# Optimization experiments

Measured on AMD Instinct MI355X. Metric: run time of the kernel, lower is better.

The kernel has to match this reference:

```python
import jax, jax.numpy as jnp
import numpy as np

D_MODEL = 1024
NUM_HEADS = 16
HEAD_DIM = D_MODEL // NUM_HEADS


def setup_inputs() -> dict:
    key = jax.random.key(0)
    ks = jax.random.split(key, 9)
    s = 1.0 / np.sqrt(D_MODEL)  # torch Linear default init range scale
    def lin(k):
        kw, kb = jax.random.split(k)
        W = jax.random.uniform(kw, (D_MODEL, D_MODEL), jnp.float32, -s, s)
        b = jax.random.uniform(kb, (D_MODEL,), jnp.float32, -s, s)
        return W, b
    Wq, bq = lin(ks[0])
    Wk, bk = lin(ks[1])
    Wv, bv = lin(ks[2])
    Wo, bo = lin(ks[3])
    x = jax.random.normal(ks[4], (4, 2048, D_MODEL), jnp.float32)
    return {"x": x, "Wq": Wq, "bq": bq, "Wk": Wk, "bk": bk,
            "Wv": Wv, "bv": bv, "Wo": Wo, "bo": bo}


def reference(x, Wq, bq, Wk, bk, Wv, bv, Wo, bo):
    B, S, _ = x.shape
    H, Dh = NUM_HEADS, HEAD_DIM
    scale = Dh ** -0.5
    # projections; W stored as [in, out] so y = x @ W + b
    q = (x @ Wq + bq).reshape(B, S, H, Dh).transpose(0, 2, 1, 3)  # [B,H,S,Dh]
    k = (x @ Wk + bk).reshape(B, S, H, Dh).transpose(0, 2, 1, 3)
    v = (x @ Wv + bv).reshape(B, S, H, Dh).transpose(0, 2, 1, 3)
    scores = jnp.einsum('bhqd,bhkd->bhqk', q, k) * scale  # [B,H,S,S]
    causal = jnp.tril(jnp.ones((S, S), dtype=bool))
    scores = jnp.where(causal[None, None], scores, jnp.finfo(scores.dtype).min)
    attn = jax.nn.softmax(scores, axis=-1)
    out = jnp.einsum('bhqk,bhkd->bhqd', attn, v)  # [B,H,S,Dh]
    out = out.transpose(0, 2, 1, 3).reshape(B, S, H * Dh)
    return out @ Wo + bo
```

## Files before the change

### kernel.cpp

```cpp
#include <hip/hip_runtime.h>
#include <math.h>

#define DM 1024
#define NH 16
#define DH 64
#define BB 4
#define SS 2048
#define MROWS (BB*SS)

typedef __bf16 bf16;
typedef __bf16 bf16x2 __attribute__((ext_vector_type(2)));
typedef __bf16 bf16x8 __attribute__((ext_vector_type(8)));
typedef float floatx4 __attribute__((ext_vector_type(4)));
typedef float floatx16 __attribute__((ext_vector_type(16)));
typedef unsigned int uintx4 __attribute__((ext_vector_type(4)));
typedef unsigned int uintx2 __attribute__((ext_vector_type(2)));

#if __has_builtin(__builtin_amdgcn_exp2f)
#define EXP2F __builtin_amdgcn_exp2f
#else
#define EXP2F exp2f
#endif

#define QSCALE (0.125f * 1.44269504088896f)

__device__ __forceinline__ void cp16(void* lds, const void* g) {
  __builtin_amdgcn_global_load_lds(
      (__attribute__((address_space(1))) void*)(void*)g,
      (__attribute__((address_space(3))) void*)lds,
      16, 0, 0);
}

__device__ __forceinline__ unsigned pk2(float a, float b) {
  bf16x2 t;
  t[0] = (bf16)a;
  t[1] = (bf16)b;
  return __builtin_bit_cast(unsigned, t);
}

#if __has_builtin(__builtin_amdgcn_permlane32_swap)
__device__ __forceinline__ void pl32(unsigned& a, unsigned& b) {
  uintx2 r = __builtin_amdgcn_permlane32_swap(a, b, false, false);
  a = r[0]; b = r[1];
}
#else
__device__ __forceinline__ void pl32(unsigned& a, unsigned& b) {
  asm volatile("v_permlane32_swap_b32 %0, %1" : "+v"(a), "+v"(b));
}
#endif

__global__ __launch_bounds__(256) void cvt_x(
    const float* __restrict__ X, bf16* __restrict__ Y) {
  int i = (blockIdx.x * 256 + threadIdx.x) * 8;
  float4 a = *(const float4*)&X[i];
  float4 b = *(const float4*)&X[i + 4];
  bf16x8 o;
  o[0] = (bf16)a.x; o[1] = (bf16)a.y; o[2] = (bf16)a.z; o[3] = (bf16)a.w;
  o[4] = (bf16)b.x; o[5] = (bf16)b.y; o[6] = (bf16)b.z; o[7] = (bf16)b.w;
  *(bf16x8*)&Y[i] = o;
}

__global__ __launch_bounds__(1024) void wtransc(
    const float* __restrict__ W0, const float* __restrict__ W1,
    const float* __restrict__ W2, const float* __restrict__ W3,
    bf16* __restrict__ T0, bf16* __restrict__ T1,
    bf16* __restrict__ T2, bf16* __restrict__ T3) {
  __shared__ float tile[32][33];
  const float* W; bf16* T;
  int z = blockIdx.z;
  if (z == 0)      { W = W0; T = T0; }
  else if (z == 1) { W = W1; T = T1; }
  else if (z == 2) { W = W2; T = T2; }
  else             { W = W3; T = T3; }
  int tx = threadIdx.x, ty = threadIdx.y;
  tile[ty][tx] = W[(blockIdx.y * 32 + ty) * DM + blockIdx.x * 32 + tx];
  __syncthreads();
  T[(blockIdx.x * 32 + ty) * DM + blockIdx.y * 32 + tx] = (bf16)tile[tx][ty];
}

#define BK 32

__global__ __launch_bounds__(512, 1) void gemm_qkv(
    const bf16* __restrict__ A, const bf16* __restrict__ WT,
    const float* __restrict__ bq, const float* __restrict__ bk,
    const float* __restrict__ bv,
    bf16* __restrict__ qb, bf16* __restrict__ kb, bf16* __restrict__ vt) {
  __shared__ __align__(16) char smem[(2 * 256 * 64 + 2 * 128 * 64) * 2];
  bf16* Ab = (bf16*)smem;
  bf16* Bb = (bf16*)(smem + 2 * 256 * 64 * 2);
  bf16* Ts = (bf16*)smem;

  int tid = threadIdx.x;
  int lane = tid & 63, w = tid >> 6;
  int wr = w >> 1, wc = w & 1;
  int qd = lane >> 4, l15 = lane & 15;

  int bid = blockIdx.x;
  int xcd = bid & 7, local = bid >> 3;
  int nb = local >> 2;
  int mb = xcd * 4 + (local & 3);
  int m0 = mb * 256;
  int n0 = nb * 128;
  int which = n0 >> 10;

  floatx4 acc[4][4] = {};

  auto stageA = [&](int pb, int t, int hf) {
    for (int i = 0; i < 2; ++i) {
      int L = i * 512 + tid;
      int row = L >> 3, ch = L & 7;
      int sch = ch ^ (row & 7);
      cp16(&Ab[pb * 256 * 64 + (hf * 128 + row) * 64 + ch * 8],
           &A[(size_t)(m0 + hf * 128 + row) * DM + t * 64 + sch * 8]);
    }
  };
  auto stageB = [&](int pb, int t) {
    for (int i = 0; i < 2; ++i) {
      int L = i * 512 + tid;
      int row = L >> 3, ch = L & 7;
      int sch = ch ^ (row & 7);
      cp16(&Bb[pb * 128 * 64 + row * 64 + ch * 8],
           &WT[(size_t)(n0 + row) * DM + t * 64 + sch * 8]);
    }
  };
  auto ldA = [&](int pb, int mt, int ks) -> bf16x8 {
    int row = wr * 64 + mt * 16 + l15;
    int c = ((ks << 2) + qd) ^ (row & 7);
    return *(const bf16x8*)&Ab[pb * 256 * 64 + row * 64 + c * 8];
  };
  auto ldB = [&](int pb, int nt, int ks) -> bf16x8 {
    int row = wc * 64 + nt * 16 + l15;
    int c = ((ks << 2) + qd) ^ (row & 7);
    return *(const bf16x8*)&Bb[pb * 128 * 64 + row * 64 + c * 8];
  };

  stageA(0, 0, 0);
  stageA(0, 0, 1);
  stageB(0, 0);
  stageB(1, 1);
  asm volatile("s_waitcnt vmcnt(2)" ::: "memory");
  __builtin_amdgcn_s_barrier();

  for (int g = 0; g < 16; ++g) {
    int pb = g & 1;
    bf16x8 af0[2][2], bfr[4][2];
    for (int mt = 0; mt < 2; ++mt)
      for (int ks = 0; ks < 2; ++ks) af0[mt][ks] = ldA(pb, mt, ks);
    for (int nt = 0; nt < 4; ++nt)
      for (int ks = 0; ks < 2; ++ks) bfr[nt][ks] = ldB(pb, nt, ks);
    if (g + 1 < 16) { stageA(pb ^ 1, g + 1, 0); stageA(pb ^ 1, g + 1, 1); }
    __builtin_amdgcn_s_barrier();
    asm volatile("s_waitcnt lgkmcnt(0)" ::: "memory");
    __builtin_amdgcn_sched_barrier(0);
    __builtin_amdgcn_s_setprio(1);
    for (int mt = 0; mt < 2; ++mt)
      for (int nt = 0; nt < 4; ++nt)
        for (int ks = 0; ks < 2; ++ks)
          acc[mt][nt] = __builtin_amdgcn_mfma_f32_16x16x32_bf16(
              af0[mt][ks], bfr[nt][ks], acc[mt][nt], 0, 0, 0);
    __builtin_amdgcn_s_setprio(0);
    __builtin_amdgcn_s_barrier();
    bf16x8 af1[2][2];
    for (int mt = 0; mt < 2; ++mt)
      for (int ks = 0; ks < 2; ++ks) af1[mt][ks] = ldA(pb, 2 + mt, ks);
    if (g + 2 < 16) stageB(pb, g + 2);
    __builtin_amdgcn_s_barrier();
    asm volatile("s_waitcnt lgkmcnt(0)" ::: "memory");
    __builtin_amdgcn_sched_barrier(0);
    __builtin_amdgcn_s_setprio(1);
    for (int mt = 0; mt < 2; ++mt)
      for (int nt = 0; nt < 4; ++nt)
        for (int ks = 0; ks < 2; ++ks)
          acc[2 + mt][nt] = __builtin_amdgcn_mfma_f32_16x16x32_bf16(
              af1[mt][ks], bfr[nt][ks], acc[2 + mt][nt], 0, 0, 0);
    __builtin_amdgcn_s_setprio(0);
    if (g < 14)
      asm volatile("s_waitcnt vmcnt(2)" ::: "memory");
    else if (g == 14)
      asm volatile("s_waitcnt vmcnt(0)" ::: "memory");
    __builtin_amdgcn_s_barrier();
  }

  __syncthreads();

  const float* bias = (which == 0) ? bq : (which == 1) ? bk : bv;

  if (which == 2) {
    for (int nt = 0; nt < 4; ++nt) {
      int dl = wc * 64 + nt * 16 + l15;
      float bv_ = bias[(n0 & 1023) + dl];
      for (int mt = 0; mt < 4; ++mt)
        for (int r = 0; r < 4; ++r)
          Ts[dl * 264 + wr * 64 + mt * 16 + qd * 4 + r] =
              (bf16)(acc[mt][nt][r] + bv_);
    }
    __syncthreads();
    int dl = tid >> 2, s0 = (tid & 3) * 64;
    size_t vrow = (size_t)((n0 & 1023) + dl) * MROWS + m0 + s0;
    for (int j = 0; j < 8; ++j)
      *(bf16x8*)&vt[vrow + j * 8] = *(const bf16x8*)&Ts[dl * 264 + s0 + j * 8];
  } else {
    bf16* out = (which == 0) ? qb : kb;
    float sc = (which == 0) ? QSCALE : 1.0f;
    for (int nt = 0; nt < 4; ++nt) {
      int col = (n0 & 1023) + wc * 64 + nt * 16 + l15;
      float bv_ = bias[col];
      for (int mt = 0; mt < 4; ++mt)
        for (int r = 0; r < 4; ++r) {
          int row = m0 + wr * 64 + mt * 16 + qd * 4 + r;
          out[(size_t)row * DM + col] = (bf16)((acc[mt][nt][r] + bv_) * sc);
        }
    }
  }
}

__global__ __launch_bounds__(512, 1) void gemm_out(
    const bf16* __restrict__ A, const bf16* __restrict__ WT,
    const float* __restrict__ bias, float* __restrict__ C) {
  __shared__ __align__(16) char smem[(2 * 256 * 64 + 2 * 128 * 64) * 2];
  bf16* Ab = (bf16*)smem;
  bf16* Bb = (bf16*)(smem + 2 * 256 * 64 * 2);

  int tid = threadIdx.x;
  int lane = tid & 63, w = tid >> 6;
  int wr = w >> 1, wc = w & 1;
  int qd = lane >> 4, l15 = lane & 15;

  int bid = blockIdx.x;
  int m0 = (bid >> 3) * 256;
  int n0 = (bid & 7) * 128;

  floatx4 acc[4][4] = {};

  auto stageA = [&](int pb, int t, int hf) {
    for (int i = 0; i < 2; ++i) {
      int L = i * 512 + tid;
      int row = L >> 3, ch = L & 7;
      int sch = ch ^ (row & 7);
      cp16(&Ab[pb * 256 * 64 + (hf * 128 + row) * 64 + ch * 8],
           &A[(size_t)(m0 + hf * 128 + row) * DM + t * 64 + sch * 8]);
    }
  };
  auto stageB = [&](int pb, int t) {
    for (int i = 0; i < 2; ++i) {
      int L = i * 512 + tid;
      int row = L >> 3, ch = L & 7;
      int sch = ch ^ (row & 7);
      cp16(&Bb[pb * 128 * 64 + row * 64 + ch * 8],
           &WT[(size_t)(n0 + row) * DM + t * 64 + sch * 8]);
    }
  };
  auto ldA = [&](int pb, int mt, int ks) -> bf16x8 {
    int row = wr * 64 + mt * 16 + l15;
    int c = ((ks << 2) + qd) ^ (row & 7);
    return *(const bf16x8*)&Ab[pb * 256 * 64 + row * 64 + c * 8];
  };
  auto ldB = [&](int pb, int nt, int ks) -> bf16x8 {
    int row = wc * 64 + nt * 16 + l15;
    int c = ((ks << 2) + qd) ^ (row & 7);
    return *(const bf16x8*)&Bb[pb * 128 * 64 + row * 64 + c * 8];
  };

  stageA(0, 0, 0);
  stageA(0, 0, 1);
  stageB(0, 0);
  stageB(1, 1);
  asm volatile("s_waitcnt vmcnt(2)" ::: "memory");
  __builtin_amdgcn_s_barrier();

  for (int g = 0; g < 16; ++g) {
    int pb = g & 1;
    bf16x8 af0[2][2], bfr[4][2];
    for (int mt = 0; mt < 2; ++mt)
      for (int ks = 0; ks < 2; ++ks) af0[mt][ks] = ldA(pb, mt, ks);
    for (int nt = 0; nt < 4; ++nt)
      for (int ks = 0; ks < 2; ++ks) bfr[nt][ks] = ldB(pb, nt, ks);
    if (g + 1 < 16) { stageA(pb ^ 1, g + 1, 0); stageA(pb ^ 1, g + 1, 1); }
    __builtin_amdgcn_s_barrier();
    asm volatile("s_waitcnt lgkmcnt(0)" ::: "memory");
    __builtin_amdgcn_sched_barrier(0);
    __builtin_amdgcn_s_setprio(1);
    for (int mt = 0; mt < 2; ++mt)
      for (int nt = 0; nt < 4; ++nt)
        for (int ks = 0; ks < 2; ++ks)
          acc[mt][nt] = __builtin_amdgcn_mfma_f32_16x16x32_bf16(
              af0[mt][ks], bfr[nt][ks], acc[mt][nt], 0, 0, 0);
    __builtin_amdgcn_s_setprio(0);
    __builtin_amdgcn_s_barrier();
    bf16x8 af1[2][2];
    for (int mt = 0; mt < 2; ++mt)
      for (int ks = 0; ks < 2; ++ks) af1[mt][ks] = ldA(pb, 2 + mt, ks);
    if (g + 2 < 16) stageB(pb, g + 2);
    __builtin_amdgcn_s_barrier();
    asm volatile("s_waitcnt lgkmcnt(0)" ::: "memory");
    __builtin_amdgcn_sched_barrier(0);
    __builtin_amdgcn_s_setprio(1);
    for (int mt = 0; mt < 2; ++mt)
      for (int nt = 0; nt < 4; ++nt)
        for (int ks = 0; ks < 2; ++ks)
          acc[2 + mt][nt] = __builtin_amdgcn_mfma_f32_16x16x32_bf16(
              af1[mt][ks], bfr[nt][ks], acc[2 + mt][nt], 0, 0, 0);
    __builtin_amdgcn_s_setprio(0);
    if (g < 14)
      asm volatile("s_waitcnt vmcnt(2)" ::: "memory");
    else if (g == 14)
      asm volatile("s_waitcnt vmcnt(0)" ::: "memory");
    __builtin_amdgcn_s_barrier();
  }

  for (int nt = 0; nt < 4; ++nt) {
    int col = n0 + wc * 64 + nt * 16 + l15;
    float bv_ = bias[col];
    for (int mt = 0; mt < 4; ++mt)
      for (int r = 0; r < 4; ++r) {
        int row = m0 + wr * 64 + mt * 16 + qd * 4 + r;
        C[(size_t)row * DM + col] = acc[mt][nt][r] + bv_;
      }
  }
}

__global__ __launch_bounds__(256, 2) void attn_fwd(
    const bf16* __restrict__ Qg, const bf16* __restrict__ Kg,
    const bf16* __restrict__ Vt, bf16* __restrict__ O) {
  __shared__ __align__(16) bf16 Kbuf[3][64 * 64];
  __shared__ __align__(16) bf16 Vbuf[3][64 * 64];

  int tid = threadIdx.x;
  int lane = tid & 63, w = tid >> 6;
  int q31 = lane & 31, hi = lane >> 5;
  int pair = blockIdx.x, h = blockIdx.y, b = blockIdx.z;
  int base = b * SS;
  int hoff = h * DH;

  auto stage = [&](int bi, int kt) {
    int kbase = base + kt * 64;
    for (int i = 0; i < 2; ++i) {
      int c = i * 256 + tid;
      int row = c >> 3;
      int sch = (c & 7) ^ (row & 7);
      cp16(&Kbuf[bi][c * 8], &Kg[(size_t)(kbase + row) * DM + hoff + sch * 8]);
      cp16(&Vbuf[bi][c * 8],
           &Vt[(size_t)(hoff + row) * MROWS + base + kt * 64 + sch * 8]);
    }
  };

  int swz = q31 & 7;

  for (int ph = 0; ph < 2; ++ph) {
    int jt = ph ? (15 - pair) : pair;
    int q0 = jt * 128;
    int nkt = 2 * jt + 2;

    stage(0, 0);
    stage(1, 1);

    int rowq = q0 + w * 32 + q31;
    bf16x8 qf[4];
    for (int ds = 0; ds < 4; ++ds)
      qf[ds] = *(const bf16x8*)
          &Qg[(size_t)(base + rowq) * DM + hoff + ds * 16 + hi * 8];

    float lacc = 0.0f;
    floatx16 oacc0 = {}, oacc1 = {};

    asm volatile("s_waitcnt vmcnt(8)" ::: "memory");
    __builtin_amdgcn_s_barrier();

    int bi = 0;
    for (int kt = 0; kt < nkt; ++kt) {
      if (kt + 2 < nkt) stage((bi + 2) % 3, kt + 2);

      floatx16 sA = {}, sB = {};
      __builtin_amdgcn_s_setprio(1);
      for (int ds = 0; ds < 4; ++ds) {
        bf16x8 kfA = *(const bf16x8*)
            &Kbuf[bi][(q31)*64 + (((ds << 1) + hi) ^ swz) * 8];
        bf16x8 kfB = *(const bf16x8*)
            &Kbuf[bi][(32 + q31) * 64 + (((ds << 1) + hi) ^ swz) * 8];
        sA = __builtin_amdgcn_mfma_f32_32x32x16_bf16(kfA, qf[ds], sA, 0, 0, 0);
        sB = __builtin_amdgcn_mfma_f32_32x32x16_bf16(kfB, qf[ds], sB, 0, 0, 0);
      }
      __builtin_amdgcn_s_setprio(0);

      if (kt >= 2 * jt) {
#pragma unroll
        for (int r = 0; r < 16; ++r) {
          int key = kt * 64 + (r & 3) + 8 * (r >> 2) + 4 * hi;
          if (key > rowq) sA[r] = -3e38f;
          if (key + 32 > rowq) sB[r] = -3e38f;
        }
      }

      float pA[16], pB[16];
#pragma unroll
      for (int r = 0; r < 16; ++r) {
        pA[r] = EXP2F(sA[r]);
        pB[r] = EXP2F(sB[r]);
      }
      float s0 = 0.f, s1 = 0.f, s2 = 0.f, s3 = 0.f;
#pragma unroll
      for (int r = 0; r < 16; r += 2) {
        s0 += pA[r]; s1 += pA[r + 1];
        s2 += pB[r]; s3 += pB[r + 1];
      }
      lacc += (s0 + s1) + (s2 + s3);

      bf16x8 pf[4];
      {
        unsigned w0 = pk2(pA[0], pA[1]), w2 = pk2(pA[4], pA[5]);
        unsigned w1 = pk2(pA[2], pA[3]), w3 = pk2(pA[6], pA[7]);
        pl32(w0, w2); pl32(w1, w3);
        uintx4 ww; ww[0] = w0; ww[1] = w1; ww[2] = w2; ww[3] = w3;
        pf[0] = __builtin_bit_cast(bf16x8, ww);
        w0 = pk2(pA[8], pA[9]);  w2 = pk2(pA[12], pA[13]);
        w1 = pk2(pA[10], pA[11]); w3 = pk2(pA[14], pA[15]);
        pl32(w0, w2); pl32(w1, w3);
        ww[0] = w0; ww[1] = w1; ww[2] = w2; ww[3] = w3;
        pf[1] = __builtin_bit_cast(bf16x8, ww);
        w0 = pk2(pB[0], pB[1]);  w2 = pk2(pB[4], pB[5]);
        w1 = pk2(pB[2], pB[3]);  w3 = pk2(pB[6], pB[7]);
        pl32(w0, w2); pl32(w1, w3);
        ww[0] = w0; ww[1] = w1; ww[2] = w2; ww[3] = w3;
        pf[2] = __builtin_bit_cast(bf16x8, ww);
        w0 = pk2(pB[8], pB[9]);  w2 = pk2(pB[12], pB[13]);
        w1 = pk2(pB[10], pB[11]); w3 = pk2(pB[14], pB[15]);
        pl32(w0, w2); pl32(w1, w3);
        ww[0] = w0; ww[1] = w1; ww[2] = w2; ww[3] = w3;
        pf[3] = __builtin_bit_cast(bf16x8, ww);
      }

      __builtin_amdgcn_s_setprio(1);
#pragma unroll
      for (int s4 = 0; s4 < 4; ++s4) {
        bf16x8 vf0 = *(const bf16x8*)
            &Vbuf[bi][(q31)*64 + (((s4 << 1) + hi) ^ swz) * 8];
        bf16x8 vf1 = *(const bf16x8*)
            &Vbuf[bi][(32 + q31) * 64 + (((s4 << 1) + hi) ^ swz) * 8];
        oacc0 = __builtin_amdgcn_mfma_f32_32x32x16_bf16(pf[s4], vf0, oacc0, 0, 0, 0);
        oacc1 = __builtin_amdgcn_mfma_f32_32x32x16_bf16(pf[s4], vf1, oacc1, 0, 0, 0);
      }
      __builtin_amdgcn_s_setprio(0);

      int rem = nkt - 1 - kt;
      if (rem >= 2) {
        asm volatile("s_waitcnt vmcnt(8)" ::: "memory");
        __builtin_amdgcn_s_barrier();
      } else if (rem == 1) {
        asm volatile("s_waitcnt vmcnt(0)" ::: "memory");
        __builtin_amdgcn_s_barrier();
      }
      bi = (bi == 2) ? 0 : bi + 1;
    }

    __syncthreads();

    lacc += __shfl_xor(lacc, 32, 64);
#pragma unroll
    for (int r = 0; r < 16; ++r) {
      int rr = (r & 3) + 8 * (r >> 2) + 4 * hi;
      float inv = 1.0f / __shfl(lacc, rr, 64);
      size_t row = (size_t)(base + q0 + w * 32 + rr) * DM + hoff;
      O[row + q31] = (bf16)(oacc0[r] * inv);
      O[row + 32 + q31] = (bf16)(oacc1[r] * inv);
    }
  }
}

extern "C" void kernel_launch(void* const* d_in, const int* in_sizes, int n_in,
                              void* d_out, int out_size, void* d_ws, size_t ws_size,
                              hipStream_t stream) {
  const float* x  = (const float*)d_in[0];
  const float* Wq = (const float*)d_in[1];
  const float* bq = (const float*)d_in[2];
  const float* Wk = (const float*)d_in[3];
  const float* bk = (const float*)d_in[4];
  const float* Wv = (const float*)d_in[5];
  const float* bv = (const float*)d_in[6];
  const float* Wo = (const float*)d_in[7];
  const float* bo = (const float*)d_in[8];
  float* out = (float*)d_out;

  char* ws = (char*)d_ws;
  const size_t act = (size_t)MROWS * DM * sizeof(bf16);
  bf16* xb    = (bf16*)(ws);
  bf16* qb    = (bf16*)(ws + act);
  bf16* kb    = (bf16*)(ws + 2 * act);
  bf16* vt    = (bf16*)(ws + 3 * act);
  bf16* ab    = (bf16*)(ws + 4 * act);
  bf16* WqkvT = (bf16*)(ws + 5 * act);
  bf16* WoT   = WqkvT + 3 * (size_t)DM * DM;

  cvt_x<<<MROWS * DM / (256 * 8), 256, 0, stream>>>(x, xb);
  wtransc<<<dim3(32, 32, 4), dim3(32, 32), 0, stream>>>(
      Wq, Wk, Wv, Wo,
      WqkvT, WqkvT + (size_t)DM * DM, WqkvT + 2 * (size_t)DM * DM, WoT);

  gemm_qkv<<<768, 512, 0, stream>>>(
      xb, WqkvT, bq, bk, bv, qb, kb, vt);

  attn_fwd<<<dim3(8, NH, BB), 256, 0, stream>>>(qb, kb, vt, ab);

  gemm_out<<<256, 512, 0, stream>>>(ab, WoT, bo, out);
}
```

Measured before the change: 252.0 us.

## Enlarge QKV GEMM tile to 256x256 with four-phase interleaved pipeline

The QKV projection GEMM tile grows from 256x128 to 256x256, and the grid is halved from 768 to 384 blocks. Warps are rearranged into a 2x4 grid with interleaved row and column fragments. The K loop is split into four MFMA phases, each overlapping a part of the next tile's A/B loads, with revised waitcnt accounting. The goal is to raise arithmetic intensity and cut redundant A-tile global loads, at the cost of more accumulator registers and fewer blocks than CUs (384 blocks on 256 CUs gives a partial second wave).

```diff
diff --git a/kernel.cpp b/kernel.cpp
--- a/kernel.cpp
+++ b/kernel.cpp
@@ -85,25 +85,26 @@
     const float* __restrict__ bq, const float* __restrict__ bk,
     const float* __restrict__ bv,
     bf16* __restrict__ qb, bf16* __restrict__ kb, bf16* __restrict__ vt) {
-  __shared__ __align__(16) char smem[(2 * 256 * 64 + 2 * 128 * 64) * 2];
+  __shared__ __align__(16) char smem[256 * 264 * 2];
   bf16* Ab = (bf16*)smem;
-  bf16* Bb = (bf16*)(smem + 2 * 256 * 64 * 2);
+  bf16* Bb = (bf16*)smem + 2 * 256 * 64;
   bf16* Ts = (bf16*)smem;
 
   int tid = threadIdx.x;
   int lane = tid & 63, w = tid >> 6;
-  int wr = w >> 1, wc = w & 1;
+  int wr = w >> 2, wc = w & 3;
   int qd = lane >> 4, l15 = lane & 15;
+  int cs = l15 & 7;
 
   int bid = blockIdx.x;
   int xcd = bid & 7, local = bid >> 3;
   int nb = local >> 2;
   int mb = xcd * 4 + (local & 3);
   int m0 = mb * 256;
-  int n0 = nb * 128;
+  int n0 = nb * 256;
   int which = n0 >> 10;
 
-  floatx4 acc[4][4] = {};
+  floatx4 acc[8][4] = {};
 
   auto stageA = [&](int pb, int t, int hf) {
     for (int i = 0; i < 2; ++i) {
@@ -114,70 +115,120 @@
            &A[(size_t)(m0 + hf * 128 + row) * DM + t * 64 + sch * 8]);
     }
   };
-  auto stageB = [&](int pb, int t) {
+  auto stageB = [&](int pb, int t, int hf) {
     for (int i = 0; i < 2; ++i) {
       int L = i * 512 + tid;
       int row = L >> 3, ch = L & 7;
       int sch = ch ^ (row & 7);
-      cp16(&Bb[pb * 128 * 64 + row * 64 + ch * 8],
-           &WT[(size_t)(n0 + row) * DM + t * 64 + sch * 8]);
+      cp16(&Bb[pb * 256 * 64 + (hf * 128 + row) * 64 + ch * 8],
+           &WT[(size_t)(n0 + hf * 128 + row) * DM + t * 64 + sch * 8]);
     }
   };
   auto ldA = [&](int pb, int mt, int ks) -> bf16x8 {
-    int row = wr * 64 + mt * 16 + l15;
-    int c = ((ks << 2) + qd) ^ (row & 7);
+    int row = mt * 32 + wr * 16 + l15;
+    int c = ((ks << 2) + qd) ^ cs;
     return *(const bf16x8*)&Ab[pb * 256 * 64 + row * 64 + c * 8];
   };
   auto ldB = [&](int pb, int nt, int ks) -> bf16x8 {
-    int row = wc * 64 + nt * 16 + l15;
-    int c = ((ks << 2) + qd) ^ (row & 7);
-    return *(const bf16x8*)&Bb[pb * 128 * 64 + row * 64 + c * 8];
+    int row = nt * 64 + wc * 16 + l15;
+    int c = ((ks << 2) + qd) ^ cs;
+    return *(const bf16x8*)&Bb[pb * 256 * 64 + row * 64 + c * 8];
   };
 
   stageA(0, 0, 0);
+  stageB(0, 0, 0);
+  stageB(0, 0, 1);
   stageA(0, 0, 1);
-  stageB(0, 0);
-  stageB(1, 1);
-  asm volatile("s_waitcnt vmcnt(2)" ::: "memory");
+  asm volatile("s_waitcnt vmcnt(4)" ::: "memory");
   __builtin_amdgcn_s_barrier();
 
-  for (int g = 0; g < 16; ++g) {
-    int pb = g & 1;
-    bf16x8 af0[2][2], bfr[4][2];
-    for (int mt = 0; mt < 2; ++mt)
+  for (int t = 0; t < 16; ++t) {
+    int pb = t & 1;
+    bool st = t < 15;
+    bf16x8 af0[4][2], af1[4][2], bf01[2][2], bf23[2][2];
+
+#pragma unroll
+    for (int mt = 0; mt < 4; ++mt)
+#pragma unroll
       for (int ks = 0; ks < 2; ++ks) af0[mt][ks] = ldA(pb, mt, ks);
-    for (int nt = 0; nt < 4; ++nt)
-      for (int ks = 0; ks < 2; ++ks) bfr[nt][ks] = ldB(pb, nt, ks);
-    if (g + 1 < 16) { stageA(pb ^ 1, g + 1, 0); stageA(pb ^ 1, g + 1, 1); }
+#pragma unroll
+    for (int nt = 0; nt < 2; ++nt)
+#pragma unroll
+      for (int ks = 0; ks < 2; ++ks) bf01[nt][ks] = ldB(pb, nt, ks);
+    if (st) stageA(pb ^ 1, t + 1, 0);
     __builtin_amdgcn_s_barrier();
     asm volatile("s_waitcnt lgkmcnt(0)" ::: "memory");
     __builtin_amdgcn_sched_barrier(0);
     __builtin_amdgcn_s_setprio(1);
-    for (int mt = 0; mt < 2; ++mt)
-      for (int nt = 0; nt < 4; ++nt)
+#pragma unroll
+    for (int mt = 0; mt < 4; ++mt)
+#pragma unroll
+      for (int nt = 0; nt < 2; ++nt)
+#pragma unroll
         for (int ks = 0; ks < 2; ++ks)
           acc[mt][nt] = __builtin_amdgcn_mfma_f32_16x16x32_bf16(
-              af0[mt][ks], bfr[nt][ks], acc[mt][nt], 0, 0, 0);
+              af0[mt][ks], bf01[nt][ks], acc[mt][nt], 0, 0, 0);
     __builtin_amdgcn_s_setprio(0);
-    __builtin_amdgcn_s_barrier();
-    bf16x8 af1[2][2];
-    for (int mt = 0; mt < 2; ++mt)
-      for (int ks = 0; ks < 2; ++ks) af1[mt][ks] = ldA(pb, 2 + mt, ks);
-    if (g + 2 < 16) stageB(pb, g + 2);
+    if (st) asm volatile("s_waitcnt vmcnt(4)" ::: "memory");
+    else    asm volatile("s_waitcnt vmcnt(2)" ::: "memory");
+    __builtin_amdgcn_s_barrier();
+
+#pragma unroll
+    for (int nt = 0; nt < 2; ++nt)
+#pragma unroll
+      for (int ks = 0; ks < 2; ++ks) bf23[nt][ks] = ldB(pb, 2 + nt, ks);
+    if (st) stageB(pb ^ 1, t + 1, 0);
     __builtin_amdgcn_s_barrier();
     asm volatile("s_waitcnt lgkmcnt(0)" ::: "memory");
     __builtin_amdgcn_sched_barrier(0);
     __builtin_amdgcn_s_setprio(1);
-    for (int mt = 0; mt < 2; ++mt)
-      for (int nt = 0; nt < 4; ++nt)
+#pragma unroll
+    for (int mt = 0; mt < 4; ++mt)
+#pragma unroll
+      for (int nt = 0; nt < 2; ++nt)
+#pragma unroll
         for (int ks = 0; ks < 2; ++ks)
-          acc[2 + mt][nt] = __builtin_amdgcn_mfma_f32_16x16x32_bf16(
-              af1[mt][ks], bfr[nt][ks], acc[2 + mt][nt], 0, 0, 0);
+          acc[mt][2 + nt] = __builtin_amdgcn_mfma_f32_16x16x32_bf16(
+              af0[mt][ks], bf23[nt][ks], acc[mt][2 + nt], 0, 0, 0);
     __builtin_amdgcn_s_setprio(0);
-    if (g < 14)
-      asm volatile("s_waitcnt vmcnt(2)" ::: "memory");
-    else if (g == 14)
-      asm volatile("s_waitcnt vmcnt(0)" ::: "memory");
+    if (st) asm volatile("s_waitcnt vmcnt(4)" ::: "memory");
+    else    asm volatile("s_waitcnt vmcnt(0)" ::: "memory");
+    __builtin_amdgcn_s_barrier();
+
+#pragma unroll
+    for (int mt = 0; mt < 4; ++mt)
+#pragma unroll
+      for (int ks = 0; ks < 2; ++ks) af1[mt][ks] = ldA(pb, 4 + mt, ks);
+    if (st) stageB(pb ^ 1, t + 1, 1);
+    __builtin_amdgcn_s_barrier();
+    asm volatile("s_waitcnt lgkmcnt(0)" ::: "memory");
+    __builtin_amdgcn_sched_barrier(0);
+    __builtin_amdgcn_s_setprio(1);
+#pragma unroll
+    for (int mt = 0; mt < 4; ++mt)
+#pragma unroll
+      for (int nt = 0; nt < 2; ++nt)
+#pragma unroll
+        for (int ks = 0; ks < 2; ++ks)
+          acc[4 + mt][nt] = __builtin_amdgcn_mfma_f32_16x16x32_bf16(
+              af1[mt][ks], bf01[nt][ks], acc[4 + mt][nt], 0, 0, 0);
+    __builtin_amdgcn_s_setprio(0);
+    if (st) asm volatile("s_waitcnt vmcnt(4)" ::: "memory");
+    __builtin_amdgcn_s_barrier();
+
+    if (st) stageA(pb ^ 1, t + 1, 1);
+    __builtin_amdgcn_s_barrier();
+    __builtin_amdgcn_s_setprio(1);
+#pragma unroll
+    for (int mt = 0; mt < 4; ++mt)
+#pragma unroll
+      for (int nt = 0; nt < 2; ++nt)
+#pragma unroll
+        for (int ks = 0; ks < 2; ++ks)
+          acc[4 + mt][2 + nt] = __builtin_amdgcn_mfma_f32_16x16x32_bf16(
+              af1[mt][ks], bf23[nt][ks], acc[4 + mt][2 + nt], 0, 0, 0);
+    __builtin_amdgcn_s_setprio(0);
+    if (st) asm volatile("s_waitcnt vmcnt(4)" ::: "memory");
     __builtin_amdgcn_s_barrier();
   }
 
@@ -186,28 +237,35 @@
   const float* bias = (which == 0) ? bq : (which == 1) ? bk : bv;
 
   if (which == 2) {
+#pragma unroll
     for (int nt = 0; nt < 4; ++nt) {
-      int dl = wc * 64 + nt * 16 + l15;
+      int dl = nt * 64 + wc * 16 + l15;
       float bv_ = bias[(n0 & 1023) + dl];
-      for (int mt = 0; mt < 4; ++mt)
+#pragma unroll
+      for (int mt = 0; mt < 8; ++mt)
+#pragma unroll
         for (int r = 0; r < 4; ++r)
-          Ts[dl * 264 + wr * 64 + mt * 16 + qd * 4 + r] =
+          Ts[dl * 264 + mt * 32 + wr * 16 + qd * 4 + r] =
               (bf16)(acc[mt][nt][r] + bv_);
     }
     __syncthreads();
-    int dl = tid >> 2, s0 = (tid & 3) * 64;
+    int dl = tid >> 1, s0 = (tid & 1) * 128;
     size_t vrow = (size_t)((n0 & 1023) + dl) * MROWS + m0 + s0;
-    for (int j = 0; j < 8; ++j)
+#pragma unroll
+    for (int j = 0; j < 16; ++j)
       *(bf16x8*)&vt[vrow + j * 8] = *(const bf16x8*)&Ts[dl * 264 + s0 + j * 8];
   } else {
     bf16* out = (which == 0) ? qb : kb;
     float sc = (which == 0) ? QSCALE : 1.0f;
+#pragma unroll
     for (int nt = 0; nt < 4; ++nt) {
-      int col = (n0 & 1023) + wc * 64 + nt * 16 + l15;
+      int col = (n0 & 1023) + nt * 64 + wc * 16 + l15;
       float bv_ = bias[col];
-      for (int mt = 0; mt < 4; ++mt)
+#pragma unroll
+      for (int mt = 0; mt < 8; ++mt)
+#pragma unroll
         for (int r = 0; r < 4; ++r) {
-          int row = m0 + wr * 64 + mt * 16 + qd * 4 + r;
+          int row = m0 + mt * 32 + wr * 16 + qd * 4 + r;
           out[(size_t)row * DM + col] = (bf16)((acc[mt][nt][r] + bv_) * sc);
         }
     }
@@ -495,7 +553,7 @@
       Wq, Wk, Wv, Wo,
       WqkvT, WqkvT + (size_t)DM * DM, WqkvT + 2 * (size_t)DM * DM, WoT);
 
-  gemm_qkv<<<768, 512, 0, stream>>>(
+  gemm_qkv<<<384, 512, 0, stream>>>(
       xb, WqkvT, bq, bk, bv, qb, kb, vt);
 
   attn_fwd<<<dim3(8, NH, BB), 256, 0, stream>>>(qb, kb, vt, ab);
```

After: 256.5 us. About the same (+1.8%).
